# Kernel optimization log

Measured on AMD Instinct MI355X. Metric: run time of the kernel, lower is better.

Reference implementation:

```python
import jax, jax.numpy as jnp
import numpy as np

INPUT_DIM = 1024
OUTPUT_DIM = 1024
DOWN = INPUT_DIM // 8  # reduction_factor=8
NUM_TOKENS = 2


def setup_inputs() -> dict:
    key = jax.random.key(0)
    k1, k2, k3, k4, k5 = jax.random.split(key, 5)
    B, Sx, Sy = 32, 2048, 512
    x = jax.random.normal(k1, (B, Sx, INPUT_DIM), dtype=jnp.float32)
    y = jax.random.normal(k2, (B, Sy, INPUT_DIM), dtype=jnp.float32)
    # nn.Parameter(torch.rand(...)) -> uniform [0,1)
    latent_tokens = jax.random.uniform(k3, (NUM_TOKENS, INPUT_DIM), dtype=jnp.float32)
    gate = jnp.zeros((1,), dtype=jnp.float32)
    # Conv1d kernel_size=1, no bias == pointwise matmul; kaiming-uniform-ish init
    lim_d = 1.0 / np.sqrt(INPUT_DIM)
    lim_u = 1.0 / np.sqrt(DOWN)
    W_down = jax.random.uniform(k4, (DOWN, INPUT_DIM), dtype=jnp.float32, minval=-lim_d, maxval=lim_d)
    W_up = jax.random.uniform(k5, (OUTPUT_DIM, DOWN), dtype=jnp.float32, minval=-lim_u, maxval=lim_u)
    return {"x": x, "y": y, "latent_tokens": latent_tokens, "gate": gate,
            "W_down": W_down, "W_up": W_up}


def reference(x, y, latent_tokens, gate, W_down, W_up):
    # tokens attend over y:  [B,T,Sy] softmax over Sy
    att_y2t = jax.nn.softmax(jnp.einsum('td,bsd->bts', latent_tokens, y), axis=-1)
    tokens = latent_tokens[None] + jnp.einsum('bts,bsd->btd', att_y2t, y)  # [B,T,D]
    # x attends over tokens: [B,Sx,T] softmax over T
    att_t2x = jax.nn.softmax(jnp.einsum('bsd,btd->bst', x, tokens), axis=-1)
    x_res = jnp.einsum('bst,btd->bsd', att_t2x, tokens)
    x = x + gate * x_res
    # 1x1 conv bottleneck: down -> ReLU -> up (pointwise matmuls)
    z = jax.nn.relu(jnp.einsum('bsd,ed->bse', x, W_down))
    out = jnp.einsum('bse,oe->bso', z, W_up)
    return out
```

## Files before the change

kernel.cpp:

```cpp
#include <hip/hip_runtime.h>
#include <hip/hip_bf16.h>

#define B_N 32
#define SX 2048
#define SY 512
#define DIM 1024
#define NTOK 2
#define DN 128
#define ODIM 1024

#define BM 128
#define BK 64

typedef __bf16 bf16;
typedef __bf16 bf16x8 __attribute__((ext_vector_type(8)));
typedef __bf16 bf16x4 __attribute__((ext_vector_type(4)));
typedef float f32x4 __attribute__((ext_vector_type(4)));

__device__ __forceinline__ f32x4 mfma16(bf16x8 a, bf16x8 b, f32x4 c) {
  return __builtin_amdgcn_mfma_f32_16x16x32_bf16(a, b, c, 0, 0, 0);
}

__global__ __launch_bounds__(256) void prep_kernel(const float* __restrict__ Wd,
                                                   const float* __restrict__ Wu,
                                                   bf16* __restrict__ wdb,
                                                   bf16* __restrict__ wub) {
  int i = blockIdx.x * 256 + threadIdx.x;
  if (i < DN * DIM) {
    wdb[i] = (bf16)Wd[i];
    wub[i] = (bf16)Wu[i];
  }
}

__global__ __launch_bounds__(256) void tokens_kernel(const float* __restrict__ y,
                                                     const float* __restrict__ lat,
                                                     const float* __restrict__ gate,
                                                     float* __restrict__ tokens) {
  if (gate[0] == 0.0f) return;
  __shared__ float s_lat[NTOK][DIM];
  __shared__ float s_sc[NTOK][SY];
  int b = blockIdx.x;
  int tid = threadIdx.x, wave = tid >> 6, lane = tid & 63;
  const float* yb = y + (size_t)b * SY * DIM;
  for (int i = tid; i < NTOK * DIM; i += 256) ((float*)s_lat)[i] = lat[i];
  __syncthreads();
  for (int s = wave * 128; s < wave * 128 + 128; ++s) {
    const float* yr = yb + (size_t)s * DIM;
    float d0 = 0.f, d1 = 0.f;
#pragma unroll
    for (int i = 0; i < 4; ++i) {
      f32x4 v = *(const f32x4*)(yr + lane * 4 + i * 256);
      f32x4 l0 = *(const f32x4*)(&s_lat[0][lane * 4 + i * 256]);
      f32x4 l1 = *(const f32x4*)(&s_lat[1][lane * 4 + i * 256]);
      d0 += v[0] * l0[0] + v[1] * l0[1] + v[2] * l0[2] + v[3] * l0[3];
      d1 += v[0] * l1[0] + v[1] * l1[1] + v[2] * l1[2] + v[3] * l1[3];
    }
#pragma unroll
    for (int off = 32; off > 0; off >>= 1) {
      d0 += __shfl_xor(d0, off);
      d1 += __shfl_xor(d1, off);
    }
    if (lane == 0) { s_sc[0][s] = d0; s_sc[1][s] = d1; }
  }
  __syncthreads();
  if (wave < 2) {
    float m = -3.4e38f;
    for (int s = lane; s < SY; s += 64) m = fmaxf(m, s_sc[wave][s]);
#pragma unroll
    for (int off = 32; off > 0; off >>= 1) m = fmaxf(m, __shfl_xor(m, off));
    float sum = 0.f;
    for (int s = lane; s < SY; s += 64) {
      float e = expf(s_sc[wave][s] - m);
      s_sc[wave][s] = e;
      sum += e;
    }
#pragma unroll
    for (int off = 32; off > 0; off >>= 1) sum += __shfl_xor(sum, off);
    float inv = 1.f / sum;
    for (int s = lane; s < SY; s += 64) s_sc[wave][s] *= inv;
  }
  __syncthreads();
  float a0[4] = {0.f, 0.f, 0.f, 0.f}, a1[4] = {0.f, 0.f, 0.f, 0.f};
  for (int s = 0; s < SY; ++s) {
    float p0 = s_sc[0][s], p1 = s_sc[1][s];
    const float* yr = yb + (size_t)s * DIM;
#pragma unroll
    for (int i = 0; i < 4; ++i) {
      float v = yr[tid + i * 256];
      a0[i] += p0 * v;
      a1[i] += p1 * v;
    }
  }
  float* tb = tokens + (size_t)b * NTOK * DIM;
#pragma unroll
  for (int i = 0; i < 4; ++i) {
    tb[tid + i * 256] = s_lat[0][tid + i * 256] + a0[i];
    tb[DIM + tid + i * 256] = s_lat[1][tid + i * 256] + a1[i];
  }
}

__global__ __launch_bounds__(512, 4) void main_kernel(const float* __restrict__ x,
                                                      const float* __restrict__ gate,
                                                      const float* __restrict__ tokens,
                                                      const bf16* __restrict__ wdb,
                                                      const bf16* __restrict__ wub,
                                                      float* __restrict__ out) {
  __shared__ union {
    bf16 xs[2][BM][BK];
    bf16 zs[BM][DN];
  } u;
  __shared__ float s_tok[NTOK][DIM];
  __shared__ float s_c[BM][2];

  int tid = threadIdx.x, w = tid >> 6, lane = tid & 63;
  int lq = lane >> 4, lr = lane & 15;
  size_t m0 = (size_t)blockIdx.x * BM;
  const float* xb = x + m0 * DIM;
  float g = gate[0];

  if (g != 0.f) {
    int b = (int)(m0 / SX);
    const float* tokb = tokens + (size_t)b * NTOK * DIM;
    for (int i = tid; i < NTOK * DIM; i += 512) ((float*)s_tok)[i] = tokb[i];
    __syncthreads();
    for (int i = 0; i < 16; ++i) {
      int r = w * 16 + i;
      const float* xrow = xb + (size_t)r * DIM;
      float d0 = 0.f, d1 = 0.f;
#pragma unroll
      for (int c = 0; c < 4; ++c) {
        f32x4 v = *(const f32x4*)(xrow + lane * 4 + c * 256);
        f32x4 t0 = *(const f32x4*)(&s_tok[0][lane * 4 + c * 256]);
        f32x4 t1 = *(const f32x4*)(&s_tok[1][lane * 4 + c * 256]);
        d0 += v[0] * t0[0] + v[1] * t0[1] + v[2] * t0[2] + v[3] * t0[3];
        d1 += v[0] * t1[0] + v[1] * t1[1] + v[2] * t1[2] + v[3] * t1[3];
      }
#pragma unroll
      for (int off = 32; off > 0; off >>= 1) {
        d0 += __shfl_xor(d0, off);
        d1 += __shfl_xor(d1, off);
      }
      if (lane == 0) {
        float mm = fmaxf(d0, d1);
        float e0 = expf(d0 - mm), e1 = expf(d1 - mm);
        float inv = g / (e0 + e1);
        s_c[r][0] = e0 * inv;
        s_c[r][1] = e1 * inv;
      }
    }
    __syncthreads();
  }

  int prow = tid >> 4;
  int pc4 = tid & 15;
  char* xsb = (char*)u.xs;

  auto loadpre = [&](f32x4 pre[4], int kcd) {
#pragma unroll
    for (int it = 0; it < 4; ++it) {
      int row = prow + it * 32;
      pre[it] = *(const f32x4*)(xb + (size_t)row * DIM + kcd * BK + pc4 * 4);
    }
  };
  auto stage = [&](char* buf, int kcd, const f32x4 pre[4]) {
    if (g != 0.f) {
      int kbase = kcd * BK + pc4 * 4;
      f32x4 t0 = *(const f32x4*)(&s_tok[0][kbase]);
      f32x4 t1 = *(const f32x4*)(&s_tok[1][kbase]);
#pragma unroll
      for (int it = 0; it < 4; ++it) {
        int row = prow + it * 32;
        float c0 = s_c[row][0], c1 = s_c[row][1];
        bf16x4 o;
#pragma unroll
        for (int j = 0; j < 4; ++j) o[j] = (bf16)(pre[it][j] + c0 * t0[j] + c1 * t1[j]);
        *(bf16x4*)(buf + row * (BK * 2) + ((pc4 * 8) ^ ((row & 7) << 4))) = o;
      }
    } else {
#pragma unroll
      for (int it = 0; it < 4; ++it) {
        int row = prow + it * 32;
        bf16x4 o;
#pragma unroll
        for (int j = 0; j < 4; ++j) o[j] = (bf16)pre[it][j];
        *(bf16x4*)(buf + row * (BK * 2) + ((pc4 * 8) ^ ((row & 7) << 4))) = o;
      }
    }
  };

  f32x4 acc1[8] = {};
  const bf16* wdw = wdb + (size_t)(w * 16 + lr) * DIM + lq * 8;

  f32x4 pre[4];
  loadpre(pre, 0);
  stage(xsb, 0, pre);
  loadpre(pre, 1);
  __syncthreads();

  for (int kc = 0; kc < DIM / BK; ++kc) {
    if (kc + 1 < DIM / BK) {
      stage(xsb + ((kc + 1) & 1) * (BM * BK * 2), kc + 1, pre);
      if (kc + 2 < DIM / BK) loadpre(pre, kc + 2);
    }
    char* buf = xsb + (kc & 1) * (BM * BK * 2);
#pragma unroll
    for (int kk = 0; kk < BK; kk += 32) {
      bf16x8 bw = *(const bf16x8*)(wdw + kc * BK + kk);
#pragma unroll
      for (int mt = 0; mt < 8; ++mt) {
        int r = mt * 16 + lr;
        bf16x8 ax = *(const bf16x8*)(buf + r * (BK * 2) + ((2 * (kk + lq * 8)) ^ ((r & 7) << 4)));
        acc1[mt] = mfma16(ax, bw, acc1[mt]);
      }
    }
    __syncthreads();
  }

  char* zsb = (char*)u.zs;
#pragma unroll
  for (int mt = 0; mt < 8; ++mt) {
#pragma unroll
    for (int reg = 0; reg < 4; ++reg) {
      int row = mt * 16 + lq * 4 + reg;
      int dn = w * 16 + lr;
      float zv = fmaxf(acc1[mt][reg], 0.f);
      *(bf16*)(zsb + row * (DN * 2) + ((2 * dn) ^ ((row & 7) << 4))) = (bf16)zv;
    }
  }
  __syncthreads();

  float* ob = out + m0 * ODIM;
#pragma unroll
  for (int half = 0; half < 2; ++half) {
    int oc0 = w * 128 + half * 64;
    bf16x8 bw2[4][4];
#pragma unroll
    for (int nt = 0; nt < 4; ++nt)
#pragma unroll
      for (int kkt = 0; kkt < 4; ++kkt)
        bw2[nt][kkt] = *(const bf16x8*)(wub + (size_t)(oc0 + nt * 16 + lr) * DN + kkt * 32 + lq * 8);
#pragma unroll
    for (int mt = 0; mt < 8; ++mt) {
      int r = mt * 16 + lr;
      bf16x8 az[4];
#pragma unroll
      for (int kkt = 0; kkt < 4; ++kkt)
        az[kkt] = *(const bf16x8*)(zsb + r * (DN * 2) + ((2 * (kkt * 32 + lq * 8)) ^ ((r & 7) << 4)));
      f32x4 a2[4] = {};
#pragma unroll
      for (int nt = 0; nt < 4; ++nt)
#pragma unroll
        for (int kkt = 0; kkt < 4; ++kkt)
          a2[nt] = mfma16(az[kkt], bw2[nt][kkt], a2[nt]);
#pragma unroll
      for (int nt = 0; nt < 4; ++nt) {
        int col = oc0 + nt * 16 + lr;
#pragma unroll
        for (int reg = 0; reg < 4; ++reg)
          ob[(size_t)(mt * 16 + lq * 4 + reg) * ODIM + col] = a2[nt][reg];
      }
    }
  }
}

extern "C" void kernel_launch(void* const* d_in, const int* in_sizes, int n_in,
                              void* d_out, int out_size, void* d_ws, size_t ws_size,
                              hipStream_t stream) {
  const float* x = (const float*)d_in[0];
  const float* y = (const float*)d_in[1];
  const float* lat = (const float*)d_in[2];
  const float* gate = (const float*)d_in[3];
  const float* Wd = (const float*)d_in[4];
  const float* Wu = (const float*)d_in[5];
  float* out = (float*)d_out;
  char* ws = (char*)d_ws;

  float* tokens = (float*)ws;
  bf16* wdb = (bf16*)(ws + 262144);
  bf16* wub = (bf16*)(ws + 524288);

  prep_kernel<<<(DN * DIM + 255) / 256, 256, 0, stream>>>(Wd, Wu, wdb, wub);
  tokens_kernel<<<B_N, 256, 0, stream>>>(y, lat, gate, tokens);
  main_kernel<<<(B_N * SX) / BM, 512, 0, stream>>>(x, gate, tokens, wdb, wub, out);
}
```

Baseline: 176.5 us.

## Load x directly into MFMA fragments, dropping LDS staging of x tiles

Rewrites the main fused kernel to use 64-row tiles with 256 threads. Each wave now reads fp32 x straight from global memory into registers, converts it to bf16 operands and double-buffers the next chunk in registers, so the shared-memory staging and per-chunk barriers are gone. The second GEMM swaps operand roles so each lane writes contiguous float4 output, replacing scattered scalar stores. Risks include less reuse of the W_down fragments across rows, more global load instructions, and an unchanged gate path that still loops over rows w*16+i even though the tile now has 64 rows.

```diff
diff --git a/kernel.cpp b/kernel.cpp
--- a/kernel.cpp
+++ b/kernel.cpp
@@ -8,9 +8,7 @@
 #define NTOK 2
 #define DN 128
 #define ODIM 1024
-
-#define BM 128
-#define BK 64
+#define BM 64
 
 typedef __bf16 bf16;
 typedef __bf16 bf16x8 __attribute__((ext_vector_type(8)));
@@ -99,29 +97,28 @@
   }
 }
 
-__global__ __launch_bounds__(512, 4) void main_kernel(const float* __restrict__ x,
+__global__ __launch_bounds__(256, 4) void main_kernel(const float* __restrict__ x,
                                                       const float* __restrict__ gate,
                                                       const float* __restrict__ tokens,
                                                       const bf16* __restrict__ wdb,
                                                       const bf16* __restrict__ wub,
                                                       float* __restrict__ out) {
-  __shared__ union {
-    bf16 xs[2][BM][BK];
-    bf16 zs[BM][DN];
-  } u;
+  __shared__ bf16 zs_raw[BM * DN];
   __shared__ float s_tok[NTOK][DIM];
   __shared__ float s_c[BM][2];
 
   int tid = threadIdx.x, w = tid >> 6, lane = tid & 63;
   int lq = lane >> 4, lr = lane & 15;
+  int wr = w >> 1, wc = w & 1;
   size_t m0 = (size_t)blockIdx.x * BM;
   const float* xb = x + m0 * DIM;
   float g = gate[0];
 
+  float c0m[2] = {0.f, 0.f}, c1m[2] = {0.f, 0.f};
   if (g != 0.f) {
     int b = (int)(m0 / SX);
     const float* tokb = tokens + (size_t)b * NTOK * DIM;
-    for (int i = tid; i < NTOK * DIM; i += 512) ((float*)s_tok)[i] = tokb[i];
+    for (int i = tid; i < NTOK * DIM; i += 256) ((float*)s_tok)[i] = tokb[i];
     __syncthreads();
     for (int i = 0; i < 16; ++i) {
       int r = w * 16 + i;
@@ -149,117 +146,116 @@
       }
     }
     __syncthreads();
-  }
-
-  int prow = tid >> 4;
-  int pc4 = tid & 15;
-  char* xsb = (char*)u.xs;
-
-  auto loadpre = [&](f32x4 pre[4], int kcd) {
-#pragma unroll
-    for (int it = 0; it < 4; ++it) {
-      int row = prow + it * 32;
-      pre[it] = *(const f32x4*)(xb + (size_t)row * DIM + kcd * BK + pc4 * 4);
-    }
+#pragma unroll
+    for (int mt = 0; mt < 2; ++mt) {
+      c0m[mt] = s_c[wr * 32 + mt * 16 + lr][0];
+      c1m[mt] = s_c[wr * 32 + mt * 16 + lr][1];
+    }
+  }
+
+  const float* xrow[2];
+  const bf16* wdp[4];
+#pragma unroll
+  for (int mt = 0; mt < 2; ++mt)
+    xrow[mt] = xb + (size_t)(wr * 32 + mt * 16 + lr) * DIM + lq * 8;
+#pragma unroll
+  for (int nf = 0; nf < 4; ++nf)
+    wdp[nf] = wdb + (size_t)(wc * 64 + nf * 16 + lr) * DIM + lq * 8;
+
+  f32x4 acc[4][2] = {};
+  f32x4 xA[2][2], xB[2][2];
+
+#pragma unroll
+  for (int mt = 0; mt < 2; ++mt) {
+    xA[mt][0] = *(const f32x4*)(xrow[mt]);
+    xA[mt][1] = *(const f32x4*)(xrow[mt] + 4);
+  }
+
+  auto phase = [&](f32x4(&cur)[2][2], f32x4(&nxt)[2][2], int kc, bool pf) {
+    if (pf) {
+#pragma unroll
+      for (int mt = 0; mt < 2; ++mt) {
+        nxt[mt][0] = *(const f32x4*)(xrow[mt] + (kc + 1) * 32);
+        nxt[mt][1] = *(const f32x4*)(xrow[mt] + (kc + 1) * 32 + 4);
+      }
+    }
+    bf16x8 wdf[4];
+#pragma unroll
+    for (int nf = 0; nf < 4; ++nf) wdf[nf] = *(const bf16x8*)(wdp[nf] + kc * 32);
+    bf16x8 bx[2];
+    if (g != 0.f) {
+      f32x4 t0a = *(const f32x4*)(&s_tok[0][kc * 32 + lq * 8]);
+      f32x4 t0b = *(const f32x4*)(&s_tok[0][kc * 32 + lq * 8 + 4]);
+      f32x4 t1a = *(const f32x4*)(&s_tok[1][kc * 32 + lq * 8]);
+      f32x4 t1b = *(const f32x4*)(&s_tok[1][kc * 32 + lq * 8 + 4]);
+#pragma unroll
+      for (int mt = 0; mt < 2; ++mt)
+#pragma unroll
+        for (int j = 0; j < 4; ++j) {
+          bx[mt][j] = (bf16)(cur[mt][0][j] + c0m[mt] * t0a[j] + c1m[mt] * t1a[j]);
+          bx[mt][4 + j] = (bf16)(cur[mt][1][j] + c0m[mt] * t0b[j] + c1m[mt] * t1b[j]);
+        }
+    } else {
+#pragma unroll
+      for (int mt = 0; mt < 2; ++mt)
+#pragma unroll
+        for (int j = 0; j < 4; ++j) {
+          bx[mt][j] = (bf16)cur[mt][0][j];
+          bx[mt][4 + j] = (bf16)cur[mt][1][j];
+        }
+    }
+#pragma unroll
+    for (int nf = 0; nf < 4; ++nf)
+#pragma unroll
+      for (int mt = 0; mt < 2; ++mt)
+        acc[nf][mt] = mfma16(wdf[nf], bx[mt], acc[nf][mt]);
   };
-  auto stage = [&](char* buf, int kcd, const f32x4 pre[4]) {
-    if (g != 0.f) {
-      int kbase = kcd * BK + pc4 * 4;
-      f32x4 t0 = *(const f32x4*)(&s_tok[0][kbase]);
-      f32x4 t1 = *(const f32x4*)(&s_tok[1][kbase]);
-#pragma unroll
-      for (int it = 0; it < 4; ++it) {
-        int row = prow + it * 32;
-        float c0 = s_c[row][0], c1 = s_c[row][1];
-        bf16x4 o;
-#pragma unroll
-        for (int j = 0; j < 4; ++j) o[j] = (bf16)(pre[it][j] + c0 * t0[j] + c1 * t1[j]);
-        *(bf16x4*)(buf + row * (BK * 2) + ((pc4 * 8) ^ ((row & 7) << 4))) = o;
-      }
-    } else {
-#pragma unroll
-      for (int it = 0; it < 4; ++it) {
-        int row = prow + it * 32;
-        bf16x4 o;
-#pragma unroll
-        for (int j = 0; j < 4; ++j) o[j] = (bf16)pre[it][j];
-        *(bf16x4*)(buf + row * (BK * 2) + ((pc4 * 8) ^ ((row & 7) << 4))) = o;
-      }
-    }
-  };
-
-  f32x4 acc1[8] = {};
-  const bf16* wdw = wdb + (size_t)(w * 16 + lr) * DIM + lq * 8;
-
-  f32x4 pre[4];
-  loadpre(pre, 0);
-  stage(xsb, 0, pre);
-  loadpre(pre, 1);
-  __syncthreads();
-
-  for (int kc = 0; kc < DIM / BK; ++kc) {
-    if (kc + 1 < DIM / BK) {
-      stage(xsb + ((kc + 1) & 1) * (BM * BK * 2), kc + 1, pre);
-      if (kc + 2 < DIM / BK) loadpre(pre, kc + 2);
-    }
-    char* buf = xsb + (kc & 1) * (BM * BK * 2);
-#pragma unroll
-    for (int kk = 0; kk < BK; kk += 32) {
-      bf16x8 bw = *(const bf16x8*)(wdw + kc * BK + kk);
-#pragma unroll
-      for (int mt = 0; mt < 8; ++mt) {
-        int r = mt * 16 + lr;
-        bf16x8 ax = *(const bf16x8*)(buf + r * (BK * 2) + ((2 * (kk + lq * 8)) ^ ((r & 7) << 4)));
-        acc1[mt] = mfma16(ax, bw, acc1[mt]);
-      }
-    }
-    __syncthreads();
-  }
-
-  char* zsb = (char*)u.zs;
-#pragma unroll
-  for (int mt = 0; mt < 8; ++mt) {
-#pragma unroll
-    for (int reg = 0; reg < 4; ++reg) {
-      int row = mt * 16 + lq * 4 + reg;
-      int dn = w * 16 + lr;
-      float zv = fmaxf(acc1[mt][reg], 0.f);
-      *(bf16*)(zsb + row * (DN * 2) + ((2 * dn) ^ ((row & 7) << 4))) = (bf16)zv;
-    }
-  }
-  __syncthreads();
+
+  for (int kc2 = 0; kc2 < 16; ++kc2) {
+    phase(xA, xB, 2 * kc2, true);
+    phase(xB, xA, 2 * kc2 + 1, kc2 < 15);
+  }
+
+  char* zb = (char*)zs_raw;
+#pragma unroll
+  for (int nf = 0; nf < 4; ++nf)
+#pragma unroll
+    for (int mt = 0; mt < 2; ++mt) {
+      int row = wr * 32 + mt * 16 + lr;
+      int dnb = wc * 128 + nf * 32 + lq * 8;
+      bf16x4 pk;
+#pragma unroll
+      for (int r = 0; r < 4; ++r) pk[r] = (bf16)fmaxf(acc[nf][mt][r], 0.f);
+      *(bf16x4*)(zb + row * 256 + (dnb ^ ((row & 7) << 4))) = pk;
+    }
+  __syncthreads();
+
+  bf16x8 zF[4][4];
+#pragma unroll
+  for (int mt = 0; mt < 4; ++mt)
+#pragma unroll
+    for (int kkt = 0; kkt < 4; ++kkt) {
+      int row = mt * 16 + lr;
+      zF[mt][kkt] = *(const bf16x8*)(zb + row * 256 + ((kkt * 64 + lq * 16) ^ ((row & 7) << 4)));
+    }
 
   float* ob = out + m0 * ODIM;
-#pragma unroll
-  for (int half = 0; half < 2; ++half) {
-    int oc0 = w * 128 + half * 64;
-    bf16x8 bw2[4][4];
-#pragma unroll
-    for (int nt = 0; nt < 4; ++nt)
-#pragma unroll
-      for (int kkt = 0; kkt < 4; ++kkt)
-        bw2[nt][kkt] = *(const bf16x8*)(wub + (size_t)(oc0 + nt * 16 + lr) * DN + kkt * 32 + lq * 8);
-#pragma unroll
-    for (int mt = 0; mt < 8; ++mt) {
-      int r = mt * 16 + lr;
-      bf16x8 az[4];
-#pragma unroll
-      for (int kkt = 0; kkt < 4; ++kkt)
-        az[kkt] = *(const bf16x8*)(zsb + r * (DN * 2) + ((2 * (kkt * 32 + lq * 8)) ^ ((r & 7) << 4)));
-      f32x4 a2[4] = {};
-#pragma unroll
-      for (int nt = 0; nt < 4; ++nt)
-#pragma unroll
-        for (int kkt = 0; kkt < 4; ++kkt)
-          a2[nt] = mfma16(az[kkt], bw2[nt][kkt], a2[nt]);
-#pragma unroll
-      for (int nt = 0; nt < 4; ++nt) {
-        int col = oc0 + nt * 16 + lr;
-#pragma unroll
-        for (int reg = 0; reg < 4; ++reg)
-          ob[(size_t)(mt * 16 + lq * 4 + reg) * ODIM + col] = a2[nt][reg];
-      }
-    }
+#pragma unroll 2
+  for (int oc16 = 0; oc16 < 16; ++oc16) {
+    int base = w * 256 + oc16 * 16;
+    bf16x8 wu[4];
+#pragma unroll
+    for (int kkt = 0; kkt < 4; ++kkt)
+      wu[kkt] = *(const bf16x8*)(wub + (size_t)(base + lr) * DN + kkt * 32 + lq * 8);
+    f32x4 a2[4] = {};
+#pragma unroll
+    for (int kkt = 0; kkt < 4; ++kkt)
+#pragma unroll
+      for (int mt = 0; mt < 4; ++mt)
+        a2[mt] = mfma16(wu[kkt], zF[mt][kkt], a2[mt]);
+#pragma unroll
+    for (int mt = 0; mt < 4; ++mt)
+      *(f32x4*)(ob + (size_t)(mt * 16 + lr) * ODIM + base + lq * 4) = a2[mt];
   }
 }
 
@@ -281,5 +277,5 @@
 
   prep_kernel<<<(DN * DIM + 255) / 256, 256, 0, stream>>>(Wd, Wu, wdb, wub);
   tokens_kernel<<<B_N, 256, 0, stream>>>(y, lat, gate, tokens);
-  main_kernel<<<(B_N * SX) / BM, 512, 0, stream>>>(x, gate, tokens, wdb, wub, out);
-}
+  main_kernel<<<(B_N * SX) / BM, 256, 0, stream>>>(x, gate, tokens, wdb, wub, out);
+}
```

After: 222.3 us. 1.26x slower.
